# Optimization experiments

Hardware: AMD Instinct MI355X
Metric: run time of the kernel (lower is better)

## Reference

```python
import jax, jax.numpy as jnp
import numpy as np

M, H, W, D = 32, 64, 64, 256
WH, WW = 8, 8          # window sizes
SH, SW = 4, 4          # shift sizes (window // 2)
NH = 8                 # attention heads
NEG = -1e9             # stands in for -inf in the swin shift mask
NW = (H // WH) * (W // WW)
WS = WH * WW


def _window_partition(x):
    # [m, H, W, d] -> [m*nw, ws, d]
    m, d = x.shape[0], x.shape[-1]
    x = x.reshape(m, H // WH, WH, W // WW, WW, d)
    x = x.transpose(0, 1, 3, 2, 4, 5)
    return x.reshape(m * NW, WS, d)


def _window_reverse(x):
    # [m*nw, ws, d] -> [m, H, W, d]
    d = x.shape[-1]
    m = x.shape[0] // NW
    x = x.reshape(m, H // WH, W // WW, WH, WW, d)
    x = x.transpose(0, 1, 3, 2, 4, 5)
    return x.reshape(m, H, W, d)


def _shift_mask():
    # static swin attention mask, built once with numpy: [nw, ws, ws]
    img = np.zeros((H, W), np.int32)
    cnt = 0
    for hs in (slice(0, -WH), slice(-WH, -SH), slice(-SH, None)):
        for ws_ in (slice(0, -WW), slice(-WW, -SW), slice(-SW, None)):
            img[hs, ws_] = cnt
            cnt += 1
    mw = img.reshape(H // WH, WH, W // WW, WW).transpose(0, 2, 1, 3).reshape(NW, WS)
    diff = mw[:, None, :] - mw[:, :, None]
    return jnp.asarray(np.where(diff != 0, NEG, 0.0).astype(np.float32))


def _mhsa(x, w_qkv, b_qkv, w_o, b_o, mask):
    # x: [B, S, D]; mask: None or [B, S, S] additive
    B, S, _ = x.shape
    hd = D // NH
    qkv = x @ w_qkv + b_qkv                       # [B, S, 3D]
    q, k, v = jnp.split(qkv, 3, axis=-1)
    q = q.reshape(B, S, NH, hd)
    k = k.reshape(B, S, NH, hd)
    v = v.reshape(B, S, NH, hd)
    scores = jnp.einsum('bqhd,bkhd->bhqk', q, k) / jnp.sqrt(jnp.float32(hd))
    if mask is not None:
        scores = scores + mask[:, None, :, :]
    attn = jax.nn.softmax(scores, axis=-1)
    out = jnp.einsum('bhqk,bkhd->bqhd', attn, v).reshape(B, S, D)
    return out @ w_o + b_o


def setup_inputs() -> dict:
    key = jax.random.key(0)
    ks = jax.random.split(key, 4)
    return {
        'x': jax.random.normal(ks[0], (M, H, W, D), jnp.float32),
        'w_qkv': 0.02 * jax.random.normal(ks[1], (D, 3 * D), jnp.float32),
        'b_qkv': jnp.zeros((3 * D,), jnp.float32),
        'w_o': 0.02 * jax.random.normal(ks[2], (D, D), jnp.float32),
        'b_o': jnp.zeros((D,), jnp.float32),
    }


def reference(x, w_qkv, b_qkv, w_o, b_o):
    m = x.shape[0]
    # pass 1: unshifted windows (grid divides evenly -> no padding, no mask)
    y = _mhsa(_window_partition(x), w_qkv, b_qkv, w_o, b_o, None)
    y = _window_reverse(y)
    # pass 2: shifted windows with swin mask
    ys = jnp.roll(y, shift=(-SH, -SW), axis=(1, 2))
    mask = jnp.broadcast_to(_shift_mask()[None], (m, NW, WS, WS)).reshape(m * NW, WS, WS)
    ys = _mhsa(_window_partition(ys), w_qkv, b_qkv, w_o, b_o, mask)
    ys = _window_reverse(ys)
    return jnp.roll(ys, shift=(SH, SW), axis=(1, 2))
```

## Files before the change

kernel.cpp:

```cpp
#include <hip/hip_runtime.h>
#include <hip/hip_bf16.h>


typedef short short8 __attribute__((ext_vector_type(8)));
typedef float floatx4 __attribute__((ext_vector_type(4)));

#define SCALE 0.17677669529663687f
#define NEGM  -1e9f

__device__ __forceinline__ void win_coords(int pass, int gw, int s,
                                           int& m, int& h, int& w) {
  m = gw >> 6;
  int wy = (gw >> 3) & 7, wx = gw & 7;
  h = wy * 8 + (s >> 3);
  w = wx * 8 + (s & 7);
  if (pass) { h = (h + 4) & 63; w = (w + 4) & 63; }
}

__device__ __forceinline__ int region_id(int wy, int wx, int s) {
  int rh = (wy == 7) ? (((s >> 3) >= 4) ? 2 : 1) : 0;
  int rw = (wx == 7) ? (((s & 7) >= 4) ? 2 : 1) : 0;
  return rh * 3 + rw;
}

__device__ __forceinline__ ushort f2b(float f) {
  uint u = __float_as_uint(f);
  return (ushort)((u + 0x7FFFu + ((u >> 16) & 1u)) >> 16);
}

__global__ __launch_bounds__(256) void wtrans_kernel(
    const float* __restrict__ wqkv, const float* __restrict__ wo,
    ushort* __restrict__ wqkvT, ushort* __restrict__ woT) {
  const int t = threadIdx.x, b = blockIdx.x;
  if (b < 768) {
    wqkvT[b * 256 + t] = f2b(wqkv[t * 768 + b]);
  } else {
    const int n = b - 768;
    woT[n * 256 + t] = f2b(wo[t * 256 + n]);
  }
}

__global__ __launch_bounds__(256) void convert_kernel(
    const float* __restrict__ src, ushort* __restrict__ xw, int pass) {
  const int t = threadIdx.x;
  const int row = blockIdx.x * 8 + (t >> 5);
  const int c = (t & 31) * 8;
  int m, h, w;
  win_coords(pass, row >> 6, row & 63, m, h, w);
  const float* s = src + (size_t)((m * 64 + h) * 64 + w) * 256 + c;
  float4 a = *(const float4*)s;
  float4 b = *(const float4*)(s + 4);
  ushort o[8] = {f2b(a.x), f2b(a.y), f2b(a.z), f2b(a.w),
                 f2b(b.x), f2b(b.y), f2b(b.z), f2b(b.w)};
  *(uint4*)(xw + (size_t)row * 256 + c) = *(uint4*)o;
}

__global__ __launch_bounds__(256, 2) void qkvattn_kernel(
    const ushort* __restrict__ xw, const ushort* __restrict__ wqkvT,
    const float* __restrict__ bqkv, ushort* __restrict__ attn_out,
    int w0, int pass) {
  __shared__ ushort sm[4][7424];
  const int t = threadIdx.x;
  const int wv = t >> 6, lane = t & 63;
  const int quad = lane >> 4, l15 = lane & 15;
  const int wi = blockIdx.x >> 1;
  const int hh = (blockIdx.x & 1) * 4 + wv;
  const ushort* xwin = xw + (size_t)wi * 16384;
  ushort* Qs = sm[wv];
  ushort* Ks = sm[wv] + 2560;
  ushort* Vt = sm[wv] + 5120;
  ushort* Ps = sm[wv];

  floatx4 acc[4][6];
#pragma unroll
  for (int i = 0; i < 4; ++i)
#pragma unroll
    for (int j = 0; j < 6; ++j) acc[i][j] = {0.f, 0.f, 0.f, 0.f};

  const ushort* brow[6];
#pragma unroll
  for (int nt = 0; nt < 6; ++nt) {
    const int n = (nt >> 1) * 256 + hh * 32 + (nt & 1) * 16 + l15;
    brow[nt] = wqkvT + (size_t)n * 256;
  }

#pragma unroll
  for (int ks = 0; ks < 8; ++ks) {
    const int k0 = ks * 32 + quad * 8;
    short8 af[4], bf[6];
#pragma unroll
    for (int mi = 0; mi < 4; ++mi)
      af[mi] = *(const short8*)(xwin + (mi * 16 + l15) * 256 + k0);
#pragma unroll
    for (int nt = 0; nt < 6; ++nt)
      bf[nt] = *(const short8*)(brow[nt] + k0);
#pragma unroll
    for (int mi = 0; mi < 4; ++mi)
#pragma unroll
      for (int nt = 0; nt < 6; ++nt)
        acc[mi][nt] = __builtin_amdgcn_mfma_f32_16x16x32_bf16(
            af[mi], bf[nt], acc[mi][nt], 0, 0, 0);
  }

#pragma unroll
  for (int nt = 0; nt < 6; ++nt) {
    const float bias = bqkv[(nt >> 1) * 256 + hh * 32 + (nt & 1) * 16 + l15];
    const int d = (nt & 1) * 16 + l15;
#pragma unroll
    for (int mi = 0; mi < 4; ++mi)
#pragma unroll
      for (int r = 0; r < 4; ++r) {
        const int tok = mi * 16 + quad * 4 + r;
        const ushort v = f2b(acc[mi][nt][r] + bias);
        if (nt < 2)      Qs[tok * 40 + d] = v;
        else if (nt < 4) Ks[tok * 40 + d] = v;
        else             Vt[d * 72 + tok] = v;
      }
  }

  short8 qf[4], kf[4];
#pragma unroll
  for (int i = 0; i < 4; ++i) {
    qf[i] = *(const short8*)&Qs[(i * 16 + l15) * 40 + quad * 8];
    kf[i] = *(const short8*)&Ks[(i * 16 + l15) * 40 + quad * 8];
  }
  floatx4 S[4][4];
#pragma unroll
  for (int i = 0; i < 4; ++i)
#pragma unroll
    for (int j = 0; j < 4; ++j) S[i][j] = {0.f, 0.f, 0.f, 0.f};
#pragma unroll
  for (int mi = 0; mi < 4; ++mi)
#pragma unroll
    for (int nj = 0; nj < 4; ++nj)
      S[mi][nj] = __builtin_amdgcn_mfma_f32_16x16x32_bf16(
          qf[mi], kf[nj], S[mi][nj], 0, 0, 0);

  const int gw = w0 + wi;
  const int wy = (gw >> 3) & 7, wx = gw & 7;
#pragma unroll
  for (int mi = 0; mi < 4; ++mi)
#pragma unroll
    for (int nj = 0; nj < 4; ++nj)
#pragma unroll
      for (int r = 0; r < 4; ++r) S[mi][nj][r] *= SCALE;
  if (pass) {
    int ridc[4];
#pragma unroll
    for (int nj = 0; nj < 4; ++nj) ridc[nj] = region_id(wy, wx, nj * 16 + l15);
#pragma unroll
    for (int mi = 0; mi < 4; ++mi)
#pragma unroll
      for (int r = 0; r < 4; ++r) {
        const int rr = region_id(wy, wx, mi * 16 + quad * 4 + r);
#pragma unroll
        for (int nj = 0; nj < 4; ++nj)
          if (rr != ridc[nj]) S[mi][nj][r] += NEGM;
      }
  }

#pragma unroll
  for (int mi = 0; mi < 4; ++mi) {
#pragma unroll
    for (int r = 0; r < 4; ++r) {
      float mx = fmaxf(fmaxf(S[mi][0][r], S[mi][1][r]),
                       fmaxf(S[mi][2][r], S[mi][3][r]));
#pragma unroll
      for (int o = 1; o < 16; o <<= 1) mx = fmaxf(mx, __shfl_xor(mx, o));
      float sm_ = 0.f;
#pragma unroll
      for (int nj = 0; nj < 4; ++nj) {
        float e = __expf(S[mi][nj][r] - mx);
        S[mi][nj][r] = e;
        sm_ += e;
      }
#pragma unroll
      for (int o = 1; o < 16; o <<= 1) sm_ += __shfl_xor(sm_, o);
      const float inv = 1.f / sm_;
      const int row = mi * 16 + quad * 4 + r;
#pragma unroll
      for (int nj = 0; nj < 4; ++nj)
        Ps[row * 72 + nj * 16 + l15] = f2b(S[mi][nj][r] * inv);
    }
  }

  floatx4 O[4][2];
#pragma unroll
  for (int i = 0; i < 4; ++i) {
    O[i][0] = {0.f, 0.f, 0.f, 0.f};
    O[i][1] = {0.f, 0.f, 0.f, 0.f};
  }
#pragma unroll
  for (int ks = 0; ks < 2; ++ks) {
    short8 bfr[2];
#pragma unroll
    for (int n2 = 0; n2 < 2; ++n2)
      bfr[n2] = *(const short8*)&Vt[(n2 * 16 + l15) * 72 + ks * 32 + quad * 8];
#pragma unroll
    for (int mi = 0; mi < 4; ++mi) {
      short8 af = *(const short8*)&Ps[(mi * 16 + l15) * 72 + ks * 32 + quad * 8];
#pragma unroll
      for (int n2 = 0; n2 < 2; ++n2)
        O[mi][n2] = __builtin_amdgcn_mfma_f32_16x16x32_bf16(
            af, bfr[n2], O[mi][n2], 0, 0, 0);
    }
  }

  ushort* ob = attn_out + (size_t)wi * 16384 + hh * 32;
#pragma unroll
  for (int mi = 0; mi < 4; ++mi)
#pragma unroll
    for (int r = 0; r < 4; ++r) {
      const int s = mi * 16 + quad * 4 + r;
      ob[s * 256 + l15]      = f2b(O[mi][0][r]);
      ob[s * 256 + 16 + l15] = f2b(O[mi][1][r]);
    }
}

__global__ __launch_bounds__(256) void proj_mfma_kernel(
    const ushort* __restrict__ attn, const ushort* __restrict__ BT,
    const float* __restrict__ bo, float* __restrict__ out,
    int w0, int pass) {
  __shared__ ushort As[128][72];
  __shared__ ushort Bs[128][72];
  const int t = threadIdx.x;
  const int lane = t & 63, wv = t >> 6;
  const int wm = wv >> 1, wn = wv & 1;
  const int quad = lane >> 4, l15 = lane & 15;
  const int sr = t >> 1, sh = (t & 1) * 32;
  const int bn0 = blockIdx.x * 128, row0 = blockIdx.y * 128;

  floatx4 acc[4][4];
#pragma unroll
  for (int i = 0; i < 4; ++i)
#pragma unroll
    for (int j = 0; j < 4; ++j) acc[i][j] = {0.f, 0.f, 0.f, 0.f};

  const ushort* arow = attn + (size_t)(row0 + sr) * 256 + sh;
  const ushort* brow = BT + (size_t)(bn0 + sr) * 256 + sh;

  for (int kc = 0; kc < 4; ++kc) {
    const int k0 = kc * 64;
#pragma unroll
    for (int u = 0; u < 4; ++u) {
      *(uint4*)&As[sr][sh + u * 8] = *(const uint4*)(arow + k0 + u * 8);
      *(uint4*)&Bs[sr][sh + u * 8] = *(const uint4*)(brow + k0 + u * 8);
    }
    __syncthreads();
#pragma unroll
    for (int ks = 0; ks < 2; ++ks) {
      const int ko = ks * 32 + quad * 8;
      short8 af[4], bf[4];
#pragma unroll
      for (int i = 0; i < 4; ++i) {
        af[i] = *(const short8*)&As[wm * 64 + i * 16 + l15][ko];
        bf[i] = *(const short8*)&Bs[wn * 64 + i * 16 + l15][ko];
      }
#pragma unroll
      for (int mi = 0; mi < 4; ++mi)
#pragma unroll
        for (int nj = 0; nj < 4; ++nj)
          acc[mi][nj] = __builtin_amdgcn_mfma_f32_16x16x32_bf16(
              af[mi], bf[nj], acc[mi][nj], 0, 0, 0);
    }
    __syncthreads();
  }

  float bias[4];
  int ncol[4];
#pragma unroll
  for (int nj = 0; nj < 4; ++nj) {
    ncol[nj] = bn0 + wn * 64 + nj * 16 + l15;
    bias[nj] = bo[ncol[nj]];
  }
#pragma unroll
  for (int mi = 0; mi < 4; ++mi)
#pragma unroll
    for (int r = 0; r < 4; ++r) {
      const int gr = row0 + wm * 64 + mi * 16 + quad * 4 + r;
      int m, h, w;
      win_coords(pass, w0 + (gr >> 6), gr & 63, m, h, w);
      float* orow = out + (size_t)((m * 64 + h) * 64 + w) * 256;
#pragma unroll
      for (int nj = 0; nj < 4; ++nj)
        orow[ncol[nj]] = acc[mi][nj][r] + bias[nj];
    }
}

extern "C" void kernel_launch(void* const* d_in, const int* in_sizes, int n_in,
                              void* d_out, int out_size, void* d_ws, size_t ws_size,
                              hipStream_t stream) {
  (void)in_sizes; (void)n_in; (void)out_size;
  const float* x    = (const float*)d_in[0];
  const float* wqkv = (const float*)d_in[1];
  const float* bqkv = (const float*)d_in[2];
  const float* wo   = (const float*)d_in[3];
  const float* bo   = (const float*)d_in[4];
  float* out = (float*)d_out;

  ushort* wqkvT = (ushort*)d_ws;
  ushort* woT   = (ushort*)((char*)d_ws + 393216);
  ushort* xw    = (ushort*)((char*)d_ws + 524288);
  char* chunkbase = (char*)d_ws + 524288 + 67108864;
  size_t fixed = 524288 + 67108864;
  size_t rem = (ws_size > fixed) ? (ws_size - fixed) : 0;
  int S = 1;
  while (S < 1024 && (size_t)(2048 / S) * 32768 > rem) S <<= 1;
  const int CW = 2048 / S;
  ushort* attnws = (ushort*)chunkbase;

  wtrans_kernel<<<dim3(1024), dim3(256), 0, stream>>>(wqkv, wo, wqkvT, woT);

  for (int pass = 0; pass < 2; ++pass) {
    const float* src = pass ? (const float*)out : x;
    convert_kernel<<<dim3(16384), dim3(256), 0, stream>>>(src, xw, pass);
    for (int c = 0; c < S; ++c) {
      const int w0 = c * CW;
      qkvattn_kernel<<<dim3(CW * 2), dim3(256), 0, stream>>>(
          xw + (size_t)w0 * 16384, wqkvT, bqkv, attnws, w0, pass);
      proj_mfma_kernel<<<dim3(2, CW / 2), dim3(256), 0, stream>>>(
          attnws, woT, bo, out, w0, pass);
    }
  }
}
```

Measured before the change: 695.3 us.

## Fuse input conversion into attention kernel and write shifted bf16 windows from projection

Removes the separate convert kernel. In pass 0 the attention kernel reads fp32 x directly, converts it to bf16 and stages the window in swizzled LDS. The pass-0 projection now writes bf16 output straight into the shifted-window layout that pass 1 consumes, so the fp32 round trip through out is skipped. Q/K/V/P LDS buffers also get XOR-swizzled layouts to avoid bank conflicts, and occupancy is raised to 3 blocks. The trade-offs are a larger shared footprint per block, extra syncthreads, and scattered 2-byte stores in the projection epilogue.

```diff
diff --git a/kernel.cpp b/kernel.cpp
--- a/kernel.cpp
+++ b/kernel.cpp
@@ -7,6 +7,11 @@
 
 #define SCALE 0.17677669529663687f
 #define NEGM  -1e9f
+
+__device__ __forceinline__ ushort f2b(float f) {
+  uint u = __float_as_uint(f);
+  return (ushort)((u + 0x7FFFu + ((u >> 16) & 1u)) >> 16);
+}
 
 __device__ __forceinline__ void win_coords(int pass, int gw, int s,
                                            int& m, int& h, int& w) {
@@ -23,9 +28,17 @@
   return rh * 3 + rw;
 }
 
-__device__ __forceinline__ ushort f2b(float f) {
-  uint u = __float_as_uint(f);
-  return (ushort)((u + 0x7FFFu + ((u >> 16) & 1u)) >> 16);
+__device__ __forceinline__ int a_idx(int row, int g) {
+  return row * 256 + ((g ^ (row & 7)) << 3);
+}
+__device__ __forceinline__ int qk_idx(int tok, int d) {
+  return tok * 32 + ((((d >> 3) ^ (tok >> 2)) & 3) << 3) + (d & 7);
+}
+__device__ __forceinline__ int v_idx(int d, int tok) {
+  return d * 64 + ((((tok >> 3) ^ d) & 7) << 3) + (tok & 7);
+}
+__device__ __forceinline__ int p_idx(int row, int col) {
+  return row * 64 + ((((col >> 3) ^ row) & 7) << 3) + (col & 7);
 }
 
 __global__ __launch_bounds__(256) void wtrans_kernel(
@@ -40,36 +53,53 @@
   }
 }
 
-__global__ __launch_bounds__(256) void convert_kernel(
-    const float* __restrict__ src, ushort* __restrict__ xw, int pass) {
-  const int t = threadIdx.x;
-  const int row = blockIdx.x * 8 + (t >> 5);
-  const int c = (t & 31) * 8;
-  int m, h, w;
-  win_coords(pass, row >> 6, row & 63, m, h, w);
-  const float* s = src + (size_t)((m * 64 + h) * 64 + w) * 256 + c;
-  float4 a = *(const float4*)s;
-  float4 b = *(const float4*)(s + 4);
-  ushort o[8] = {f2b(a.x), f2b(a.y), f2b(a.z), f2b(a.w),
-                 f2b(b.x), f2b(b.y), f2b(b.z), f2b(b.w)};
-  *(uint4*)(xw + (size_t)row * 256 + c) = *(uint4*)o;
-}
-
-__global__ __launch_bounds__(256, 2) void qkvattn_kernel(
-    const ushort* __restrict__ xw, const ushort* __restrict__ wqkvT,
-    const float* __restrict__ bqkv, ushort* __restrict__ attn_out,
-    int w0, int pass) {
-  __shared__ ushort sm[4][7424];
+__global__ __launch_bounds__(256, 3) void qkvattn_kernel(
+    const float* __restrict__ x, const ushort* __restrict__ xwc,
+    const ushort* __restrict__ wqkvT, const float* __restrict__ bqkv,
+    ushort* __restrict__ attn_out, int w0, int pass) {
+  __shared__ ushort sm[24576];
   const int t = threadIdx.x;
   const int wv = t >> 6, lane = t & 63;
   const int quad = lane >> 4, l15 = lane & 15;
   const int wi = blockIdx.x >> 1;
   const int hh = (blockIdx.x & 1) * 4 + wv;
-  const ushort* xwin = xw + (size_t)wi * 16384;
-  ushort* Qs = sm[wv];
-  ushort* Ks = sm[wv] + 2560;
-  ushort* Vt = sm[wv] + 5120;
-  ushort* Ps = sm[wv];
+  const int gw = w0 + wi;
+
+  ushort* As = sm;
+  ushort* Qs = sm + wv * 6144;
+  ushort* Ks = Qs + 2048;
+  ushort* Vt = Qs + 4096;
+  ushort* Ps = Qs;
+
+  {
+    const int rr = t >> 5;
+    const int gg = t & 31;
+    if (pass) {
+      const ushort* src = xwc + (size_t)wi * 16384 + rr * 256 + gg * 8;
+#pragma unroll
+      for (int j = 0; j < 8; ++j) {
+        uint4 v = *(const uint4*)(src + j * 2048);
+        *(uint4*)&As[a_idx(j * 8 + rr, gg)] = v;
+      }
+    } else {
+      const int m = gw >> 6;
+      const int hb = ((gw >> 3) & 7) * 8;
+      const int w = (gw & 7) * 8 + rr;
+      const float* src = x + (size_t)((m * 64 + hb) * 64 + w) * 256 + gg * 8;
+#pragma unroll
+      for (int j = 0; j < 8; ++j) {
+        float4 a = *(const float4*)(src + (size_t)j * 16384);
+        float4 b = *(const float4*)(src + (size_t)j * 16384 + 4);
+        short8 o;
+        o[0] = (short)f2b(a.x); o[1] = (short)f2b(a.y);
+        o[2] = (short)f2b(a.z); o[3] = (short)f2b(a.w);
+        o[4] = (short)f2b(b.x); o[5] = (short)f2b(b.y);
+        o[6] = (short)f2b(b.z); o[7] = (short)f2b(b.w);
+        *(short8*)&As[a_idx(j * 8 + rr, gg)] = o;
+      }
+    }
+  }
+  __syncthreads();
 
   floatx4 acc[4][6];
 #pragma unroll
@@ -90,7 +120,7 @@
     short8 af[4], bf[6];
 #pragma unroll
     for (int mi = 0; mi < 4; ++mi)
-      af[mi] = *(const short8*)(xwin + (mi * 16 + l15) * 256 + k0);
+      af[mi] = *(const short8*)&As[a_idx(mi * 16 + l15, ks * 4 + quad)];
 #pragma unroll
     for (int nt = 0; nt < 6; ++nt)
       bf[nt] = *(const short8*)(brow[nt] + k0);
@@ -101,28 +131,30 @@
         acc[mi][nt] = __builtin_amdgcn_mfma_f32_16x16x32_bf16(
             af[mi], bf[nt], acc[mi][nt], 0, 0, 0);
   }
+  __syncthreads();
 
 #pragma unroll
   for (int nt = 0; nt < 6; ++nt) {
-    const float bias = bqkv[(nt >> 1) * 256 + hh * 32 + (nt & 1) * 16 + l15];
     const int d = (nt & 1) * 16 + l15;
+    const float bias = bqkv[(nt >> 1) * 256 + hh * 32 + d];
 #pragma unroll
     for (int mi = 0; mi < 4; ++mi)
 #pragma unroll
       for (int r = 0; r < 4; ++r) {
         const int tok = mi * 16 + quad * 4 + r;
         const ushort v = f2b(acc[mi][nt][r] + bias);
-        if (nt < 2)      Qs[tok * 40 + d] = v;
-        else if (nt < 4) Ks[tok * 40 + d] = v;
-        else             Vt[d * 72 + tok] = v;
+        if (nt < 2)      Qs[qk_idx(tok, d)] = v;
+        else if (nt < 4) Ks[qk_idx(tok, d)] = v;
+        else             Vt[v_idx(d, tok)] = v;
       }
   }
 
   short8 qf[4], kf[4];
 #pragma unroll
   for (int i = 0; i < 4; ++i) {
-    qf[i] = *(const short8*)&Qs[(i * 16 + l15) * 40 + quad * 8];
-    kf[i] = *(const short8*)&Ks[(i * 16 + l15) * 40 + quad * 8];
+    const int row = i * 16 + l15;
+    qf[i] = *(const short8*)&Qs[qk_idx(row, quad * 8)];
+    kf[i] = *(const short8*)&Ks[qk_idx(row, quad * 8)];
   }
   floatx4 S[4][4];
 #pragma unroll
@@ -136,7 +168,6 @@
       S[mi][nj] = __builtin_amdgcn_mfma_f32_16x16x32_bf16(
           qf[mi], kf[nj], S[mi][nj], 0, 0, 0);
 
-  const int gw = w0 + wi;
   const int wy = (gw >> 3) & 7, wx = gw & 7;
 #pragma unroll
   for (int mi = 0; mi < 4; ++mi)
@@ -180,7 +211,7 @@
       const int row = mi * 16 + quad * 4 + r;
 #pragma unroll
       for (int nj = 0; nj < 4; ++nj)
-        Ps[row * 72 + nj * 16 + l15] = f2b(S[mi][nj][r] * inv);
+        Ps[p_idx(row, nj * 16 + l15)] = f2b(S[mi][nj][r] * inv);
     }
   }
 
@@ -195,14 +226,14 @@
     short8 bfr[2];
 #pragma unroll
     for (int n2 = 0; n2 < 2; ++n2)
-      bfr[n2] = *(const short8*)&Vt[(n2 * 16 + l15) * 72 + ks * 32 + quad * 8];
+      bfr[n2] = *(const short8*)&Vt[v_idx(n2 * 16 + l15, ks * 32 + quad * 8)];
 #pragma unroll
     for (int mi = 0; mi < 4; ++mi) {
-      short8 af = *(const short8*)&Ps[(mi * 16 + l15) * 72 + ks * 32 + quad * 8];
+      short8 af2 = *(const short8*)&Ps[p_idx(mi * 16 + l15, ks * 32 + quad * 8)];
 #pragma unroll
       for (int n2 = 0; n2 < 2; ++n2)
         O[mi][n2] = __builtin_amdgcn_mfma_f32_16x16x32_bf16(
-            af, bfr[n2], O[mi][n2], 0, 0, 0);
+            af2, bfr[n2], O[mi][n2], 0, 0, 0);
     }
   }
 
@@ -220,7 +251,7 @@
 __global__ __launch_bounds__(256) void proj_mfma_kernel(
     const ushort* __restrict__ attn, const ushort* __restrict__ BT,
     const float* __restrict__ bo, float* __restrict__ out,
-    int w0, int pass) {
+    ushort* __restrict__ xw, int w0, int pass) {
   __shared__ ushort As[128][72];
   __shared__ ushort Bs[128][72];
   const int t = threadIdx.x;
@@ -280,10 +311,20 @@
       const int gr = row0 + wm * 64 + mi * 16 + quad * 4 + r;
       int m, h, w;
       win_coords(pass, w0 + (gr >> 6), gr & 63, m, h, w);
-      float* orow = out + (size_t)((m * 64 + h) * 64 + w) * 256;
-#pragma unroll
-      for (int nj = 0; nj < 4; ++nj)
-        orow[ncol[nj]] = acc[mi][nj][r] + bias[nj];
+      if (pass == 0) {
+        const int h2 = (h - 4) & 63, w2 = (w - 4) & 63;
+        const int row2 = ((m * 64 + (h2 >> 3) * 8 + (w2 >> 3)) << 6) +
+                         (h2 & 7) * 8 + (w2 & 7);
+        ushort* xrow = xw + (size_t)row2 * 256;
+#pragma unroll
+        for (int nj = 0; nj < 4; ++nj)
+          xrow[ncol[nj]] = f2b(acc[mi][nj][r] + bias[nj]);
+      } else {
+        float* orow = out + (size_t)((m * 64 + h) * 64 + w) * 256;
+#pragma unroll
+        for (int nj = 0; nj < 4; ++nj)
+          orow[ncol[nj]] = acc[mi][nj][r] + bias[nj];
+      }
     }
 }
 
@@ -312,14 +353,12 @@
   wtrans_kernel<<<dim3(1024), dim3(256), 0, stream>>>(wqkv, wo, wqkvT, woT);
 
   for (int pass = 0; pass < 2; ++pass) {
-    const float* src = pass ? (const float*)out : x;
-    convert_kernel<<<dim3(16384), dim3(256), 0, stream>>>(src, xw, pass);
     for (int c = 0; c < S; ++c) {
       const int w0 = c * CW;
       qkvattn_kernel<<<dim3(CW * 2), dim3(256), 0, stream>>>(
-          xw + (size_t)w0 * 16384, wqkvT, bqkv, attnws, w0, pass);
+          x, xw + (size_t)w0 * 16384, wqkvT, bqkv, attnws, w0, pass);
       proj_mfma_kernel<<<dim3(2, CW / 2), dim3(256), 0, stream>>>(
-          attnws, woT, bo, out, w0, pass);
-    }
-  }
-}
+          attnws, woT, bo, out, xw, w0, pass);
+    }
+  }
+}
```

Measured after the change: 682.5 us. Within noise of the previous version (-1.8%).

## Emit pass-one output as shifted bf16 windows and drop chunking

Applied to the files above, without the earlier changes.

The pass-0 projection epilogue now writes bf16 directly in the shifted-window layout that pass 1 consumes. This removes the second convert kernel and the full fp32 write and re-read of the intermediate tensor. The attention kernel becomes one wave per (window, head) block with XOR-swizzled shared-memory layouts to cut bank conflicts. Window chunking is removed, so the code assumes the workspace can hold the full attention buffer. When workspace is small, the shifted buffer aliases the output buffer.

```diff
diff --git a/kernel.cpp b/kernel.cpp
--- a/kernel.cpp
+++ b/kernel.cpp
@@ -7,6 +7,11 @@
 
 #define SCALE 0.17677669529663687f
 #define NEGM  -1e9f
+
+__device__ __forceinline__ ushort f2b(float f) {
+  uint u = __float_as_uint(f);
+  return (ushort)((u + 0x7FFFu + ((u >> 16) & 1u)) >> 16);
+}
 
 __device__ __forceinline__ void win_coords(int pass, int gw, int s,
                                            int& m, int& h, int& w) {
@@ -23,9 +28,14 @@
   return rh * 3 + rw;
 }
 
-__device__ __forceinline__ ushort f2b(float f) {
-  uint u = __float_as_uint(f);
-  return (ushort)((u + 0x7FFFu + ((u >> 16) & 1u)) >> 16);
+__device__ __forceinline__ int qk_idx(int tok, int d) {
+  return tok * 32 + ((((d >> 3) ^ (tok >> 2)) & 3) << 3) + (d & 7);
+}
+__device__ __forceinline__ int v_idx(int d, int tok) {
+  return d * 64 + ((((tok >> 3) ^ d) & 7) << 3) + (tok & 7);
+}
+__device__ __forceinline__ int p_idx(int row, int col) {
+  return row * 64 + ((((col >> 3) ^ row) & 7) << 3) + (col & 7);
 }
 
 __global__ __launch_bounds__(256) void wtrans_kernel(
@@ -41,12 +51,12 @@
 }
 
 __global__ __launch_bounds__(256) void convert_kernel(
-    const float* __restrict__ src, ushort* __restrict__ xw, int pass) {
+    const float* __restrict__ src, ushort* __restrict__ xw) {
   const int t = threadIdx.x;
   const int row = blockIdx.x * 8 + (t >> 5);
   const int c = (t & 31) * 8;
   int m, h, w;
-  win_coords(pass, row >> 6, row & 63, m, h, w);
+  win_coords(0, row >> 6, row & 63, m, h, w);
   const float* s = src + (size_t)((m * 64 + h) * 64 + w) * 256 + c;
   float4 a = *(const float4*)s;
   float4 b = *(const float4*)(s + 4);
@@ -55,21 +65,20 @@
   *(uint4*)(xw + (size_t)row * 256 + c) = *(uint4*)o;
 }
 
-__global__ __launch_bounds__(256, 2) void qkvattn_kernel(
+__global__ __launch_bounds__(64) void qkvattn_kernel(
     const ushort* __restrict__ xw, const ushort* __restrict__ wqkvT,
-    const float* __restrict__ bqkv, ushort* __restrict__ attn_out,
-    int w0, int pass) {
-  __shared__ ushort sm[4][7424];
-  const int t = threadIdx.x;
-  const int wv = t >> 6, lane = t & 63;
+    const float* __restrict__ bqkv, ushort* __restrict__ attn_out, int pass) {
+  __shared__ ushort sm[6144];
+  const int lane = threadIdx.x;
   const int quad = lane >> 4, l15 = lane & 15;
-  const int wi = blockIdx.x >> 1;
-  const int hh = (blockIdx.x & 1) * 4 + wv;
+  const int wi = blockIdx.x;
+  const int hh = blockIdx.y;
+  ushort* Qs = sm;
+  ushort* Ks = sm + 2048;
+  ushort* Vt = sm + 4096;
+  ushort* Ps = sm;
+
   const ushort* xwin = xw + (size_t)wi * 16384;
-  ushort* Qs = sm[wv];
-  ushort* Ks = sm[wv] + 2560;
-  ushort* Vt = sm[wv] + 5120;
-  ushort* Ps = sm[wv];
 
   floatx4 acc[4][6];
 #pragma unroll
@@ -104,25 +113,26 @@
 
 #pragma unroll
   for (int nt = 0; nt < 6; ++nt) {
-    const float bias = bqkv[(nt >> 1) * 256 + hh * 32 + (nt & 1) * 16 + l15];
     const int d = (nt & 1) * 16 + l15;
+    const float bias = bqkv[(nt >> 1) * 256 + hh * 32 + d];
 #pragma unroll
     for (int mi = 0; mi < 4; ++mi)
 #pragma unroll
       for (int r = 0; r < 4; ++r) {
         const int tok = mi * 16 + quad * 4 + r;
         const ushort v = f2b(acc[mi][nt][r] + bias);
-        if (nt < 2)      Qs[tok * 40 + d] = v;
-        else if (nt < 4) Ks[tok * 40 + d] = v;
-        else             Vt[d * 72 + tok] = v;
+        if (nt < 2)      Qs[qk_idx(tok, d)] = v;
+        else if (nt < 4) Ks[qk_idx(tok, d)] = v;
+        else             Vt[v_idx(d, tok)] = v;
       }
   }
 
   short8 qf[4], kf[4];
 #pragma unroll
   for (int i = 0; i < 4; ++i) {
-    qf[i] = *(const short8*)&Qs[(i * 16 + l15) * 40 + quad * 8];
-    kf[i] = *(const short8*)&Ks[(i * 16 + l15) * 40 + quad * 8];
+    const int row = i * 16 + l15;
+    qf[i] = *(const short8*)&Qs[qk_idx(row, quad * 8)];
+    kf[i] = *(const short8*)&Ks[qk_idx(row, quad * 8)];
   }
   floatx4 S[4][4];
 #pragma unroll
@@ -136,8 +146,7 @@
       S[mi][nj] = __builtin_amdgcn_mfma_f32_16x16x32_bf16(
           qf[mi], kf[nj], S[mi][nj], 0, 0, 0);
 
-  const int gw = w0 + wi;
-  const int wy = (gw >> 3) & 7, wx = gw & 7;
+  const int wy = (wi >> 3) & 7, wx = wi & 7;
 #pragma unroll
   for (int mi = 0; mi < 4; ++mi)
 #pragma unroll
@@ -180,7 +189,7 @@
       const int row = mi * 16 + quad * 4 + r;
 #pragma unroll
       for (int nj = 0; nj < 4; ++nj)
-        Ps[row * 72 + nj * 16 + l15] = f2b(S[mi][nj][r] * inv);
+        Ps[p_idx(row, nj * 16 + l15)] = f2b(S[mi][nj][r] * inv);
     }
   }
 
@@ -195,14 +204,14 @@
     short8 bfr[2];
 #pragma unroll
     for (int n2 = 0; n2 < 2; ++n2)
-      bfr[n2] = *(const short8*)&Vt[(n2 * 16 + l15) * 72 + ks * 32 + quad * 8];
+      bfr[n2] = *(const short8*)&Vt[v_idx(n2 * 16 + l15, ks * 32 + quad * 8)];
 #pragma unroll
     for (int mi = 0; mi < 4; ++mi) {
-      short8 af = *(const short8*)&Ps[(mi * 16 + l15) * 72 + ks * 32 + quad * 8];
+      short8 af2 = *(const short8*)&Ps[p_idx(mi * 16 + l15, ks * 32 + quad * 8)];
 #pragma unroll
       for (int n2 = 0; n2 < 2; ++n2)
         O[mi][n2] = __builtin_amdgcn_mfma_f32_16x16x32_bf16(
-            af, bfr[n2], O[mi][n2], 0, 0, 0);
+            af2, bfr[n2], O[mi][n2], 0, 0, 0);
     }
   }
 
@@ -220,7 +229,7 @@
 __global__ __launch_bounds__(256) void proj_mfma_kernel(
     const ushort* __restrict__ attn, const ushort* __restrict__ BT,
     const float* __restrict__ bo, float* __restrict__ out,
-    int w0, int pass) {
+    ushort* __restrict__ xw1, int w0, int pass) {
   __shared__ ushort As[128][72];
   __shared__ ushort Bs[128][72];
   const int t = threadIdx.x;
@@ -280,10 +289,20 @@
       const int gr = row0 + wm * 64 + mi * 16 + quad * 4 + r;
       int m, h, w;
       win_coords(pass, w0 + (gr >> 6), gr & 63, m, h, w);
-      float* orow = out + (size_t)((m * 64 + h) * 64 + w) * 256;
-#pragma unroll
-      for (int nj = 0; nj < 4; ++nj)
-        orow[ncol[nj]] = acc[mi][nj][r] + bias[nj];
+      if (pass == 0) {
+        const int h2 = (h - 4) & 63, w2 = (w - 4) & 63;
+        const int row2 = ((m * 64 + (h2 >> 3) * 8 + (w2 >> 3)) << 6) +
+                         (h2 & 7) * 8 + (w2 & 7);
+        ushort* xrow = xw1 + (size_t)row2 * 256;
+#pragma unroll
+        for (int nj = 0; nj < 4; ++nj)
+          xrow[ncol[nj]] = f2b(acc[mi][nj][r] + bias[nj]);
+      } else {
+        float* orow = out + (size_t)((m * 64 + h) * 64 + w) * 256;
+#pragma unroll
+        for (int nj = 0; nj < 4; ++nj)
+          orow[ncol[nj]] = acc[mi][nj][r] + bias[nj];
+      }
     }
 }
 
@@ -300,26 +319,27 @@
 
   ushort* wqkvT = (ushort*)d_ws;
   ushort* woT   = (ushort*)((char*)d_ws + 393216);
-  ushort* xw    = (ushort*)((char*)d_ws + 524288);
-  char* chunkbase = (char*)d_ws + 524288 + 67108864;
+  ushort* xw0   = (ushort*)((char*)d_ws + 524288);
+  char* p2 = (char*)d_ws + 524288 + 67108864;
   size_t fixed = 524288 + 67108864;
   size_t rem = (ws_size > fixed) ? (ws_size - fixed) : 0;
-  int S = 1;
-  while (S < 1024 && (size_t)(2048 / S) * 32768 > rem) S <<= 1;
-  const int CW = 2048 / S;
-  ushort* attnws = (ushort*)chunkbase;
+
+  ushort* attnws = (ushort*)p2;
+  ushort* xw1;
+  if (rem >= 2ull * 67108864) {
+    xw1 = (ushort*)(p2 + 67108864);
+  } else {
+    xw1 = (ushort*)out;
+  }
 
   wtrans_kernel<<<dim3(1024), dim3(256), 0, stream>>>(wqkv, wo, wqkvT, woT);
+  convert_kernel<<<dim3(16384), dim3(256), 0, stream>>>(x, xw0);
 
   for (int pass = 0; pass < 2; ++pass) {
-    const float* src = pass ? (const float*)out : x;
-    convert_kernel<<<dim3(16384), dim3(256), 0, stream>>>(src, xw, pass);
-    for (int c = 0; c < S; ++c) {
-      const int w0 = c * CW;
-      qkvattn_kernel<<<dim3(CW * 2), dim3(256), 0, stream>>>(
-          xw + (size_t)w0 * 16384, wqkvT, bqkv, attnws, w0, pass);
-      proj_mfma_kernel<<<dim3(2, CW / 2), dim3(256), 0, stream>>>(
-          attnws, woT, bo, out, w0, pass);
-    }
-  }
-}
+    const ushort* src = pass ? xw1 : xw0;
+    qkvattn_kernel<<<dim3(2048, 8), dim3(64), 0, stream>>>(
+        src, wqkvT, bqkv, attnws, pass);
+    proj_mfma_kernel<<<dim3(2, 1024), dim3(256), 0, stream>>>(
+        attnws, woT, bo, out, xw1, 0, pass);
+  }
+}
```

Result: slower. 834.4 us (+20.0%).

## Fuse QKV-attention and output projection per window, write shifted bf16 directly

Applied to the files above, without the earlier changes.

Combines the attention and output-projection kernels into one 512-thread block per window that handles all 8 heads, staging the concatenated head outputs in shared memory and running the projection in place. This removes the attention-output round trip through global memory and the separate projection launch. Pass 0 now writes its bf16 output straight into the shifted window layout for pass 1, which removes the fp32 write-back and the second convert kernel. It also drops the chunked workspace loop, assumes the workspace holds two full bf16 activation buffers, and uses more shared memory per block, which may lower occupancy.

```diff
diff --git a/kernel.cpp b/kernel.cpp
--- a/kernel.cpp
+++ b/kernel.cpp
@@ -7,6 +7,11 @@
 
 #define SCALE 0.17677669529663687f
 #define NEGM  -1e9f
+
+__device__ __forceinline__ ushort f2b(float f) {
+  uint u = __float_as_uint(f);
+  return (ushort)((u + 0x7FFFu + ((u >> 16) & 1u)) >> 16);
+}
 
 __device__ __forceinline__ void win_coords(int pass, int gw, int s,
                                            int& m, int& h, int& w) {
@@ -21,11 +26,6 @@
   int rh = (wy == 7) ? (((s >> 3) >= 4) ? 2 : 1) : 0;
   int rw = (wx == 7) ? (((s & 7) >= 4) ? 2 : 1) : 0;
   return rh * 3 + rw;
-}
-
-__device__ __forceinline__ ushort f2b(float f) {
-  uint u = __float_as_uint(f);
-  return (ushort)((u + 0x7FFFu + ((u >> 16) & 1u)) >> 16);
 }
 
 __global__ __launch_bounds__(256) void wtrans_kernel(
@@ -41,12 +41,12 @@
 }
 
 __global__ __launch_bounds__(256) void convert_kernel(
-    const float* __restrict__ src, ushort* __restrict__ xw, int pass) {
+    const float* __restrict__ src, ushort* __restrict__ xw) {
   const int t = threadIdx.x;
   const int row = blockIdx.x * 8 + (t >> 5);
   const int c = (t & 31) * 8;
   int m, h, w;
-  win_coords(pass, row >> 6, row & 63, m, h, w);
+  win_coords(0, row >> 6, row & 63, m, h, w);
   const float* s = src + (size_t)((m * 64 + h) * 64 + w) * 256 + c;
   float4 a = *(const float4*)s;
   float4 b = *(const float4*)(s + 4);
@@ -55,21 +55,23 @@
   *(uint4*)(xw + (size_t)row * 256 + c) = *(uint4*)o;
 }
 
-__global__ __launch_bounds__(256, 2) void qkvattn_kernel(
+__global__ __launch_bounds__(512) void fused_kernel(
     const ushort* __restrict__ xw, const ushort* __restrict__ wqkvT,
-    const float* __restrict__ bqkv, ushort* __restrict__ attn_out,
-    int w0, int pass) {
-  __shared__ ushort sm[4][7424];
+    const float* __restrict__ bqkv, const ushort* __restrict__ woT,
+    const float* __restrict__ bo, float* __restrict__ out,
+    ushort* __restrict__ xw1, int pass) {
+  __shared__ ushort sm[8][7424];
   const int t = threadIdx.x;
   const int wv = t >> 6, lane = t & 63;
   const int quad = lane >> 4, l15 = lane & 15;
-  const int wi = blockIdx.x >> 1;
-  const int hh = (blockIdx.x & 1) * 4 + wv;
+  const int wi = blockIdx.x;
+  const int hh = wv;
   const ushort* xwin = xw + (size_t)wi * 16384;
   ushort* Qs = sm[wv];
   ushort* Ks = sm[wv] + 2560;
   ushort* Vt = sm[wv] + 5120;
   ushort* Ps = sm[wv];
+  ushort* Ot = &sm[0][0];
 
   floatx4 acc[4][6];
 #pragma unroll
@@ -104,8 +106,8 @@
 
 #pragma unroll
   for (int nt = 0; nt < 6; ++nt) {
-    const float bias = bqkv[(nt >> 1) * 256 + hh * 32 + (nt & 1) * 16 + l15];
     const int d = (nt & 1) * 16 + l15;
+    const float bias = bqkv[(nt >> 1) * 256 + hh * 32 + d];
 #pragma unroll
     for (int mi = 0; mi < 4; ++mi)
 #pragma unroll
@@ -136,8 +138,7 @@
       S[mi][nj] = __builtin_amdgcn_mfma_f32_16x16x32_bf16(
           qf[mi], kf[nj], S[mi][nj], 0, 0, 0);
 
-  const int gw = w0 + wi;
-  const int wy = (gw >> 3) & 7, wx = gw & 7;
+  const int wy = (wi >> 3) & 7, wx = wi & 7;
 #pragma unroll
   for (int mi = 0; mi < 4; ++mi)
 #pragma unroll
@@ -198,99 +199,79 @@
       bfr[n2] = *(const short8*)&Vt[(n2 * 16 + l15) * 72 + ks * 32 + quad * 8];
 #pragma unroll
     for (int mi = 0; mi < 4; ++mi) {
-      short8 af = *(const short8*)&Ps[(mi * 16 + l15) * 72 + ks * 32 + quad * 8];
+      short8 af2 = *(const short8*)&Ps[(mi * 16 + l15) * 72 + ks * 32 + quad * 8];
 #pragma unroll
       for (int n2 = 0; n2 < 2; ++n2)
         O[mi][n2] = __builtin_amdgcn_mfma_f32_16x16x32_bf16(
-            af, bfr[n2], O[mi][n2], 0, 0, 0);
-    }
-  }
-
-  ushort* ob = attn_out + (size_t)wi * 16384 + hh * 32;
+            af2, bfr[n2], O[mi][n2], 0, 0, 0);
+    }
+  }
+
+  __syncthreads();
 #pragma unroll
   for (int mi = 0; mi < 4; ++mi)
 #pragma unroll
     for (int r = 0; r < 4; ++r) {
       const int s = mi * 16 + quad * 4 + r;
-      ob[s * 256 + l15]      = f2b(O[mi][0][r]);
-      ob[s * 256 + 16 + l15] = f2b(O[mi][1][r]);
-    }
-}
-
-__global__ __launch_bounds__(256) void proj_mfma_kernel(
-    const ushort* __restrict__ attn, const ushort* __restrict__ BT,
-    const float* __restrict__ bo, float* __restrict__ out,
-    int w0, int pass) {
-  __shared__ ushort As[128][72];
-  __shared__ ushort Bs[128][72];
-  const int t = threadIdx.x;
-  const int lane = t & 63, wv = t >> 6;
-  const int wm = wv >> 1, wn = wv & 1;
-  const int quad = lane >> 4, l15 = lane & 15;
-  const int sr = t >> 1, sh = (t & 1) * 32;
-  const int bn0 = blockIdx.x * 128, row0 = blockIdx.y * 128;
-
-  floatx4 acc[4][4];
-#pragma unroll
-  for (int i = 0; i < 4; ++i)
-#pragma unroll
-    for (int j = 0; j < 4; ++j) acc[i][j] = {0.f, 0.f, 0.f, 0.f};
-
-  const ushort* arow = attn + (size_t)(row0 + sr) * 256 + sh;
-  const ushort* brow = BT + (size_t)(bn0 + sr) * 256 + sh;
-
-  for (int kc = 0; kc < 4; ++kc) {
-    const int k0 = kc * 64;
-#pragma unroll
-    for (int u = 0; u < 4; ++u) {
-      *(uint4*)&As[sr][sh + u * 8] = *(const uint4*)(arow + k0 + u * 8);
-      *(uint4*)&Bs[sr][sh + u * 8] = *(const uint4*)(brow + k0 + u * 8);
-    }
-    __syncthreads();
-#pragma unroll
-    for (int ks = 0; ks < 2; ++ks) {
-      const int ko = ks * 32 + quad * 8;
-      short8 af[4], bf[4];
-#pragma unroll
-      for (int i = 0; i < 4; ++i) {
-        af[i] = *(const short8*)&As[wm * 64 + i * 16 + l15][ko];
-        bf[i] = *(const short8*)&Bs[wn * 64 + i * 16 + l15][ko];
-      }
-#pragma unroll
-      for (int mi = 0; mi < 4; ++mi)
-#pragma unroll
-        for (int nj = 0; nj < 4; ++nj)
-          acc[mi][nj] = __builtin_amdgcn_mfma_f32_16x16x32_bf16(
-              af[mi], bf[nj], acc[mi][nj], 0, 0, 0);
-    }
-    __syncthreads();
-  }
-
-  float bias[4];
-  int ncol[4];
-#pragma unroll
-  for (int nj = 0; nj < 4; ++nj) {
-    ncol[nj] = bn0 + wn * 64 + nj * 16 + l15;
-    bias[nj] = bo[ncol[nj]];
-  }
+      Ot[s * 264 + hh * 32 + l15]      = f2b(O[mi][0][r]);
+      Ot[s * 264 + hh * 32 + 16 + l15] = f2b(O[mi][1][r]);
+    }
+  __syncthreads();
+
+  floatx4 acc2[4][2];
+#pragma unroll
+  for (int i = 0; i < 4; ++i) {
+    acc2[i][0] = {0.f, 0.f, 0.f, 0.f};
+    acc2[i][1] = {0.f, 0.f, 0.f, 0.f};
+  }
+  const ushort* w0row = woT + (size_t)(hh * 32 + l15) * 256;
+  const ushort* w1row = w0row + 16 * 256;
+#pragma unroll
+  for (int ks = 0; ks < 8; ++ks) {
+    const int k0 = ks * 32 + quad * 8;
+    short8 bf0 = *(const short8*)(w0row + k0);
+    short8 bf1 = *(const short8*)(w1row + k0);
+    short8 af3[4];
+#pragma unroll
+    for (int mi = 0; mi < 4; ++mi)
+      af3[mi] = *(const short8*)&Ot[(mi * 16 + l15) * 264 + k0];
+#pragma unroll
+    for (int mi = 0; mi < 4; ++mi) {
+      acc2[mi][0] = __builtin_amdgcn_mfma_f32_16x16x32_bf16(
+          af3[mi], bf0, acc2[mi][0], 0, 0, 0);
+      acc2[mi][1] = __builtin_amdgcn_mfma_f32_16x16x32_bf16(
+          af3[mi], bf1, acc2[mi][1], 0, 0, 0);
+    }
+  }
+
+  const float bias0 = bo[hh * 32 + l15];
+  const float bias1 = bo[hh * 32 + 16 + l15];
 #pragma unroll
   for (int mi = 0; mi < 4; ++mi)
 #pragma unroll
     for (int r = 0; r < 4; ++r) {
-      const int gr = row0 + wm * 64 + mi * 16 + quad * 4 + r;
+      const int s = mi * 16 + quad * 4 + r;
       int m, h, w;
-      win_coords(pass, w0 + (gr >> 6), gr & 63, m, h, w);
-      float* orow = out + (size_t)((m * 64 + h) * 64 + w) * 256;
-#pragma unroll
-      for (int nj = 0; nj < 4; ++nj)
-        orow[ncol[nj]] = acc[mi][nj][r] + bias[nj];
+      win_coords(pass, wi, s, m, h, w);
+      if (pass == 0) {
+        const int h2 = (h - 4) & 63, w2 = (w - 4) & 63;
+        const int row2 = ((m * 64 + (h2 >> 3) * 8 + (w2 >> 3)) << 6) +
+                         (h2 & 7) * 8 + (w2 & 7);
+        ushort* xrow = xw1 + (size_t)row2 * 256;
+        xrow[hh * 32 + l15]      = f2b(acc2[mi][0][r] + bias0);
+        xrow[hh * 32 + 16 + l15] = f2b(acc2[mi][1][r] + bias1);
+      } else {
+        float* orow = out + (size_t)((m * 64 + h) * 64 + w) * 256;
+        orow[hh * 32 + l15]      = acc2[mi][0][r] + bias0;
+        orow[hh * 32 + 16 + l15] = acc2[mi][1][r] + bias1;
+      }
     }
 }
 
 extern "C" void kernel_launch(void* const* d_in, const int* in_sizes, int n_in,
                               void* d_out, int out_size, void* d_ws, size_t ws_size,
                               hipStream_t stream) {
-  (void)in_sizes; (void)n_in; (void)out_size;
+  (void)in_sizes; (void)n_in; (void)out_size; (void)ws_size;
   const float* x    = (const float*)d_in[0];
   const float* wqkv = (const float*)d_in[1];
   const float* bqkv = (const float*)d_in[2];
@@ -300,26 +281,14 @@
 
   ushort* wqkvT = (ushort*)d_ws;
   ushort* woT   = (ushort*)((char*)d_ws + 393216);
-  ushort* xw    = (ushort*)((char*)d_ws + 524288);
-  char* chunkbase = (char*)d_ws + 524288 + 67108864;
-  size_t fixed = 524288 + 67108864;
-  size_t rem = (ws_size > fixed) ? (ws_size - fixed) : 0;
-  int S = 1;
-  while (S < 1024 && (size_t)(2048 / S) * 32768 > rem) S <<= 1;
-  const int CW = 2048 / S;
-  ushort* attnws = (ushort*)chunkbase;
+  ushort* xw0   = (ushort*)((char*)d_ws + 524288);
+  ushort* xw1   = (ushort*)((char*)d_ws + 524288 + 67108864);
 
   wtrans_kernel<<<dim3(1024), dim3(256), 0, stream>>>(wqkv, wo, wqkvT, woT);
-
-  for (int pass = 0; pass < 2; ++pass) {
-    const float* src = pass ? (const float*)out : x;
-    convert_kernel<<<dim3(16384), dim3(256), 0, stream>>>(src, xw, pass);
-    for (int c = 0; c < S; ++c) {
-      const int w0 = c * CW;
-      qkvattn_kernel<<<dim3(CW * 2), dim3(256), 0, stream>>>(
-          xw + (size_t)w0 * 16384, wqkvT, bqkv, attnws, w0, pass);
-      proj_mfma_kernel<<<dim3(2, CW / 2), dim3(256), 0, stream>>>(
-          attnws, woT, bo, out, w0, pass);
-    }
-  }
-}
+  convert_kernel<<<dim3(16384), dim3(256), 0, stream>>>(x, xw0);
+
+  fused_kernel<<<dim3(2048), dim3(512), 0, stream>>>(
+      xw0, wqkvT, bqkv, woT, bo, out, xw1, 0);
+  fused_kernel<<<dim3(2048), dim3(512), 0, stream>>>(
+      xw1, wqkvT, bqkv, woT, bo, out, xw1, 1);
+}
```

Measured after the change: 704.9 us. No clear change (+1.4%).
